# Kernel optimization log

Hardware: AMD Instinct MI355X
Metric: run time of the kernel (lower is better)

## Reference

```python
import jax, jax.numpy as jnp
import numpy as np


def setup_inputs() -> dict:
    key = jax.random.key(0)
    L, N, Q, C = 6, 64, 64, 256
    hs_pair = jax.random.normal(key, (L, N, Q, C), dtype=jnp.float32)
    return {"hs_pair": hs_pair}


def _merge_step(centers):
    # centers: [L, N, Q, C] -> [L, N, Q-1, C]
    L, N, Q, C = centers.shape
    # pairwise Euclidean distance via gram matrix (avoids [L,N,Q,Q,C] diff tensor)
    sq = jnp.sum(centers * centers, axis=-1)                      # [L,N,Q]
    gram = jnp.einsum('lnqc,lnpc->lnqp', centers, centers)        # [L,N,Q,Q]
    d2 = sq[..., :, None] + sq[..., None, :] - 2.0 * gram
    dist = jnp.sqrt(jnp.maximum(d2, 0.0))                         # [L,N,Q,Q]
    dist = dist + jnp.max(dist) * jnp.eye(Q, dtype=dist.dtype)
    idx = jnp.argmin(dist.reshape(L, N, Q * Q), axis=2)           # [L,N]
    x, y = idx // Q, idx % Q                                      # row-major argmin => x < y
    cx = jnp.take_along_axis(centers, x[:, :, None, None], axis=2)[:, :, 0]  # [L,N,C]
    cy = jnp.take_along_axis(centers, y[:, :, None, None], axis=2)[:, :, 0]  # [L,N,C]
    merged = (cx + cy) * 0.5
    last = centers[:, :, -1]                                      # [L,N,C]
    qr = jnp.arange(Q)
    mask_x = (qr[None, None, :] == x[:, :, None])[..., None]      # [L,N,Q,1]
    mask_y = (qr[None, None, :] == y[:, :, None])[..., None]
    centers = jnp.where(mask_x, merged[:, :, None, :], centers)
    centers = jnp.where(mask_y, last[:, :, None, :], centers)
    return centers[:, :, :-1]


def reference(hs_pair):
    centers = hs_pair
    Q0 = centers.shape[2]
    # Q-2 sequential merges; each iteration has a distinct static shape,
    # so a Python loop (unrolled under jit) is the correct structure.
    for _ in range(Q0 - 2):
        centers = _merge_step(centers)
    return centers  # [L, N, 2, C]
```

## Files before the change

kernel.cpp:

```cpp
#include <hip/hip_runtime.h>
#include <stdint.h>

#define NSLICE 384
#define QMAX   64
#define CDIM   256
#define NTHR   512

#define SW(r,c) ((r)*QMAX + ((c)^(r)))
#define INF_F  __int_as_float(0x7F800000)

__device__ __forceinline__ float dpp_sum64(float v) {
#define DPP_ADD(c) v += __int_as_float(__builtin_amdgcn_update_dpp(0, __float_as_int(v), c, 0xf, 0xf, true))
    DPP_ADD(0x111);
    DPP_ADD(0x112);
    DPP_ADD(0x114);
    DPP_ADD(0x118);
    DPP_ADD(0x142);
    DPP_ADD(0x143);
#undef DPP_ADD
    return v;
}

template<int CTRL>
__device__ __forceinline__ unsigned dpp_min_step(unsigned v) {
    unsigned o = (unsigned)__builtin_amdgcn_update_dpp((int)v, (int)v, CTRL, 0xf, 0xf, false);
    return v < o ? v : v < o ? v : (o < v ? o : v);
}

template<int CTRL>
__device__ __forceinline__ unsigned dpp_min_step2(unsigned v) {
    unsigned o = (unsigned)__builtin_amdgcn_update_dpp((int)v, (int)v, CTRL, 0xf, 0xf, false);
    return o < v ? o : v;
}

__device__ __forceinline__ unsigned wave_min_bcast(unsigned v) {
    v = dpp_min_step2<0x111>(v);
    v = dpp_min_step2<0x112>(v);
    v = dpp_min_step2<0x114>(v);
    v = dpp_min_step2<0x118>(v);
    v = dpp_min_step2<0x142>(v);
    v = dpp_min_step2<0x143>(v);
    return (unsigned)__builtin_amdgcn_readlane((int)v, 63);
}

__device__ __forceinline__ unsigned oct_min_all(unsigned v) {
    v = dpp_min_step2<0xB1>(v);
    v = dpp_min_step2<0x4E>(v);
    v = dpp_min_step2<0x124>(v);
    return v;
}

__launch_bounds__(NTHR, 4)
__global__ void hca_kernel(const float* __restrict__ in, float* __restrict__ out) {
    __shared__ __align__(16) float cen[QMAX * CDIM];
    __shared__ __align__(16) float dist[QMAX * QMAX];
    unsigned long long* const scratch = (unsigned long long*)(dist + 63 * QMAX);

    const int tid  = threadIdx.x;
    const int lane = tid & 63;
    const int w    = tid >> 6;
    const int slice = blockIdx.x;
    const float* src = in + (size_t)slice * (QMAX * CDIM);
    float* dst = out + (size_t)slice * (2 * CDIM);

    {
        const float4* s4 = (const float4*)src;
        float4* c4 = (float4*)cen;
        #pragma unroll
        for (int i = 0; i < (QMAX * CDIM / 4) / NTHR; ++i)
            c4[tid + i * NTHR] = s4[tid + i * NTHR];
    }
    __syncthreads();

    {
        float4 A[8];
        #pragma unroll
        for (int r = 0; r < 8; ++r)
            A[r] = ((const float4*)(cen + (w + 8 * r) * CDIM))[lane];

        #pragma unroll
        for (int r = 0; r < 8; ++r) {
            float t = A[r].x * A[r].x;
            t = fmaf(A[r].y, A[r].y, t); t = fmaf(A[r].z, A[r].z, t); t = fmaf(A[r].w, A[r].w, t);
            float s = dpp_sum64(t);
            if (lane == 63) dist[(w + 8 * r) * QMAX] = s;
        }
        __syncthreads();

        float sqq[8];
        #pragma unroll
        for (int r = 0; r < 8; ++r) sqq[r] = dist[(w + 8 * r) * QMAX];
        for (int p = 1; p < QMAX; ++p) {
            const float4 b = ((const float4*)(cen + p * CDIM))[lane];
            const float sqp = dist[p * QMAX];
            #pragma unroll
            for (int r = 0; r < 8; ++r) {
                const int q = w + 8 * r;
                if (q < p) {
                    float t = A[r].x * b.x;
                    t = fmaf(A[r].y, b.y, t); t = fmaf(A[r].z, b.z, t); t = fmaf(A[r].w, b.w, t);
                    float s = dpp_sum64(t);
                    if (lane == 63) {
                        float d2 = sqq[r] + sqp - 2.0f * s;
                        float d  = sqrtf(fmaxf(d2, 0.0f));
                        dist[SW(q, p)] = d;
                        dist[SW(p, q)] = d;
                    }
                }
            }
        }
    }
    __syncthreads();

    auto chunk_min = [&](const float4& dv, unsigned& part) {
        unsigned u0 = __float_as_uint(dv.x), u1 = __float_as_uint(dv.y);
        unsigned u2 = __float_as_uint(dv.z), u3 = __float_as_uint(dv.w);
        unsigned m01 = u0 < u1 ? u0 : u1;
        unsigned m23 = u2 < u3 ? u2 : u3;
        unsigned m = m01 < m23 ? m01 : m23;
        part = part < m ? part : m;
    };
    auto chunk_idx = [&](int i, const float4& dv, unsigned g, unsigned& bi) {
        const int rr  = 4 * i + (lane >> 4);
        const int rb  = rr * 64;
        const int cc0 = (lane & 15) * 4;
        #pragma unroll
        for (int e = 0; e < 4; ++e) {
            unsigned db  = __float_as_uint((&dv.x)[e]);
            unsigned idx = (unsigned)(rb + ((cc0 + e) ^ rr));
            if (db == g) bi = idx < bi ? idx : bi;
        }
    };

    unsigned flat0, d0bits;
    {
        unsigned part = 0xFFFFFFFFu;
        float4 dv[16];
        #pragma unroll
        for (int i = 0; i < 16; ++i) {
            dv[i] = ((const float4*)dist)[i * 64 + lane];
            chunk_min(dv[i], part);
        }
        d0bits = wave_min_bcast(part);
        unsigned bi = 0xFFFFFFFFu;
        #pragma unroll
        for (int i = 0; i < 16; ++i) chunk_idx(i, dv[i], d0bits, bi);
        flat0 = wave_min_bcast(bi);
    }
    __syncthreads();

    for (int Q = QMAX; Q > 2; --Q) {
        const int Qm1 = Q - 1;

        int x = 0, y = 0;
        float dxy = 0.0f;
        if (w < 2) {
            unsigned flat, g;
            if (Q == QMAX) {
                flat = flat0; g = d0bits;
            } else {
                unsigned long long k = scratch[lane & 7];
                unsigned hi = (unsigned)(k >> 32), lo = (unsigned)k;
                g = oct_min_all(hi);
                unsigned c2 = (hi == g) ? lo : 0xFFFFFFFFu;
                flat = oct_min_all(c2);
            }
            x = (int)((flat >> 6) & 63); y = (int)(flat & 63);
            dxy = __uint_as_float(g);
        }

        if (w == 0) {
            const int p = lane;
            const bool act = (p < Qm1) && (p != x);
            const int p_old = (p == y) ? Qm1 : p;
            float dxp = 0.0f, dyp = 0.0f;
            if (act) { dxp = dist[SW(x, p_old)]; dyp = dist[SW(y, p_old)]; }
            const bool mv = (y != Qm1) && (p < Qm1) && (p != x) && (p != y);
            float rowQ1 = 0.0f, colQ1 = 0.0f;
            if (mv) { rowQ1 = dist[SW(Qm1, p)]; colQ1 = dist[SW(p, Qm1)]; }
            float t = 0.5f * (dxp * dxp + dyp * dyp) - 0.25f * (dxy * dxy);
            float d = sqrtf(fmaxf(t, 0.0f));
            if (mv) { dist[SW(y, p)] = rowQ1; dist[SW(p, y)] = colQ1; }
            if (p < Q) { dist[SW(Qm1, p)] = INF_F; dist[SW(p, Qm1)] = INF_F; }
            if (act) { dist[SW(x, p)] = d; dist[SW(p, x)] = d; }
        }
        if (w == 1) {
            const float4 cx  = ((const float4*)(cen + x * CDIM))[lane];
            const float4 cy4 = ((const float4*)(cen + y * CDIM))[lane];
            const float4 cq  = ((const float4*)(cen + Qm1 * CDIM))[lane];
            float4 m;
            m.x = (cx.x + cy4.x) * 0.5f; m.y = (cx.y + cy4.y) * 0.5f;
            m.z = (cx.z + cy4.z) * 0.5f; m.w = (cx.w + cy4.w) * 0.5f;
            ((float4*)(cen + x * CDIM))[lane] = m;
            if (y != Qm1) ((float4*)(cen + y * CDIM))[lane] = cq;
        }
        __syncthreads();

        if (Q > 3) {
            const int Qs = Q - 1;
            unsigned part = 0xFFFFFFFFu;
            float4 v0, v1;
            const bool l0 = (4 * w < Qs);
            const bool l1 = (4 * (w + 8) < Qs);
            if (l0) {
                v0 = ((const float4*)dist)[w * 64 + lane];
                chunk_min(v0, part);
            }
            if (l1) {
                v1 = ((const float4*)dist)[(w + 8) * 64 + lane];
                if (w + 8 == 15 && lane >= 48) {
                    v1.x = INF_F; v1.y = INF_F; v1.z = INF_F; v1.w = INF_F;
                }
                chunk_min(v1, part);
            }
            unsigned g = wave_min_bcast(part);
            unsigned bi = 0xFFFFFFFFu;
            if (l0) chunk_idx(w, v0, g, bi);
            if (l1) chunk_idx(w + 8, v1, g, bi);
            unsigned bidx = wave_min_bcast(bi);
            if (lane == 0) scratch[w] = ((unsigned long long)g << 32) | bidx;
        }
        __syncthreads();
    }

    for (int i = tid; i < 2 * CDIM; i += NTHR)
        dst[i] = cen[i];
}

extern "C" void kernel_launch(void* const* d_in, const int* in_sizes, int n_in,
                              void* d_out, int out_size, void* d_ws, size_t ws_size,
                              hipStream_t stream) {
    (void)in_sizes; (void)n_in; (void)d_ws; (void)ws_size; (void)out_size;
    const float* in = (const float*)d_in[0];
    float* out = (float*)d_out;
    hca_kernel<<<NSLICE, NTHR, 0, stream>>>(in, out);
}
```

Before: 127.9 us.

## Halve block to four waves and reduce candidates with scalar 64-bit min

Cuts the workgroup from 8 to 4 waves, so each wave now holds 16 rows in the Gram phase and scans 4 float4 chunks per step of the sequential argmin loop. The cross-wave combine now reads the four scratch entries as packed 64-bit keys and takes their min directly, replacing the octet DPP reductions, then broadcasts x, y and dxy with readfirstlane. The aim is to cut per-iteration barrier and reduction overhead in the 62-step serial loop, since fewer waves take part in each __syncthreads. The cost is more register pressure and more serial work per wave in the Gram phase.

```diff
diff --git a/kernel.cpp b/kernel.cpp
--- a/kernel.cpp
+++ b/kernel.cpp
@@ -4,10 +4,11 @@
 #define NSLICE 384
 #define QMAX   64
 #define CDIM   256
-#define NTHR   512
+#define NTHR   256
 
 #define SW(r,c) ((r)*QMAX + ((c)^(r)))
 #define INF_F  __int_as_float(0x7F800000)
+typedef unsigned long long ull;
 
 __device__ __forceinline__ float dpp_sum64(float v) {
 #define DPP_ADD(c) v += __int_as_float(__builtin_amdgcn_update_dpp(0, __float_as_int(v), c, 0xf, 0xf, true))
@@ -24,37 +25,24 @@
 template<int CTRL>
 __device__ __forceinline__ unsigned dpp_min_step(unsigned v) {
     unsigned o = (unsigned)__builtin_amdgcn_update_dpp((int)v, (int)v, CTRL, 0xf, 0xf, false);
-    return v < o ? v : v < o ? v : (o < v ? o : v);
-}
-
-template<int CTRL>
-__device__ __forceinline__ unsigned dpp_min_step2(unsigned v) {
-    unsigned o = (unsigned)__builtin_amdgcn_update_dpp((int)v, (int)v, CTRL, 0xf, 0xf, false);
     return o < v ? o : v;
 }
 
 __device__ __forceinline__ unsigned wave_min_bcast(unsigned v) {
-    v = dpp_min_step2<0x111>(v);
-    v = dpp_min_step2<0x112>(v);
-    v = dpp_min_step2<0x114>(v);
-    v = dpp_min_step2<0x118>(v);
-    v = dpp_min_step2<0x142>(v);
-    v = dpp_min_step2<0x143>(v);
+    v = dpp_min_step<0x111>(v);
+    v = dpp_min_step<0x112>(v);
+    v = dpp_min_step<0x114>(v);
+    v = dpp_min_step<0x118>(v);
+    v = dpp_min_step<0x142>(v);
+    v = dpp_min_step<0x143>(v);
     return (unsigned)__builtin_amdgcn_readlane((int)v, 63);
 }
 
-__device__ __forceinline__ unsigned oct_min_all(unsigned v) {
-    v = dpp_min_step2<0xB1>(v);
-    v = dpp_min_step2<0x4E>(v);
-    v = dpp_min_step2<0x124>(v);
-    return v;
-}
-
-__launch_bounds__(NTHR, 4)
+__launch_bounds__(NTHR, 2)
 __global__ void hca_kernel(const float* __restrict__ in, float* __restrict__ out) {
     __shared__ __align__(16) float cen[QMAX * CDIM];
     __shared__ __align__(16) float dist[QMAX * QMAX];
-    unsigned long long* const scratch = (unsigned long long*)(dist + 63 * QMAX);
+    ull* const scratch = (ull*)(dist + 63 * QMAX);
 
     const int tid  = threadIdx.x;
     const int lane = tid & 63;
@@ -73,29 +61,29 @@
     __syncthreads();
 
     {
-        float4 A[8];
-        #pragma unroll
-        for (int r = 0; r < 8; ++r)
-            A[r] = ((const float4*)(cen + (w + 8 * r) * CDIM))[lane];
-
-        #pragma unroll
-        for (int r = 0; r < 8; ++r) {
+        float4 A[16];
+        #pragma unroll
+        for (int r = 0; r < 16; ++r)
+            A[r] = ((const float4*)(cen + (w + 4 * r) * CDIM))[lane];
+
+        #pragma unroll
+        for (int r = 0; r < 16; ++r) {
             float t = A[r].x * A[r].x;
             t = fmaf(A[r].y, A[r].y, t); t = fmaf(A[r].z, A[r].z, t); t = fmaf(A[r].w, A[r].w, t);
             float s = dpp_sum64(t);
-            if (lane == 63) dist[(w + 8 * r) * QMAX] = s;
+            if (lane == 63) dist[(w + 4 * r) * QMAX] = s;
         }
         __syncthreads();
 
-        float sqq[8];
-        #pragma unroll
-        for (int r = 0; r < 8; ++r) sqq[r] = dist[(w + 8 * r) * QMAX];
+        float sqq[16];
+        #pragma unroll
+        for (int r = 0; r < 16; ++r) sqq[r] = dist[(w + 4 * r) * QMAX];
         for (int p = 1; p < QMAX; ++p) {
             const float4 b = ((const float4*)(cen + p * CDIM))[lane];
             const float sqp = dist[p * QMAX];
             #pragma unroll
-            for (int r = 0; r < 8; ++r) {
-                const int q = w + 8 * r;
+            for (int r = 0; r < 16; ++r) {
+                const int q = w + 4 * r;
                 if (q < p) {
                     float t = A[r].x * b.x;
                     t = fmaf(A[r].y, b.y, t); t = fmaf(A[r].z, b.z, t); t = fmaf(A[r].w, b.w, t);
@@ -155,18 +143,20 @@
         int x = 0, y = 0;
         float dxy = 0.0f;
         if (w < 2) {
-            unsigned flat, g;
+            ull kmin;
             if (Q == QMAX) {
-                flat = flat0; g = d0bits;
+                kmin = ((ull)d0bits << 32) | flat0;
             } else {
-                unsigned long long k = scratch[lane & 7];
-                unsigned hi = (unsigned)(k >> 32), lo = (unsigned)k;
-                g = oct_min_all(hi);
-                unsigned c2 = (hi == g) ? lo : 0xFFFFFFFFu;
-                flat = oct_min_all(c2);
+                ull s0 = scratch[0], s1 = scratch[1], s2 = scratch[2], s3 = scratch[3];
+                ull a0 = s0 < s1 ? s0 : s1;
+                ull a1 = s2 < s3 ? s2 : s3;
+                kmin = a0 < a1 ? a0 : a1;
             }
-            x = (int)((flat >> 6) & 63); y = (int)(flat & 63);
-            dxy = __uint_as_float(g);
+            const unsigned fl = (unsigned)kmin & 0xFFFu;
+            x = __builtin_amdgcn_readfirstlane((int)(fl >> 6));
+            y = __builtin_amdgcn_readfirstlane((int)(fl & 63u));
+            dxy = __uint_as_float(
+                (unsigned)__builtin_amdgcn_readfirstlane((int)(unsigned)(kmin >> 32)));
         }
 
         if (w == 0) {
@@ -199,32 +189,34 @@
         if (Q > 3) {
             const int Qs = Q - 1;
             unsigned part = 0xFFFFFFFFu;
-            float4 v0, v1;
-            const bool l0 = (4 * w < Qs);
-            const bool l1 = (4 * (w + 8) < Qs);
-            if (l0) {
-                v0 = ((const float4*)dist)[w * 64 + lane];
-                chunk_min(v0, part);
-            }
-            if (l1) {
-                v1 = ((const float4*)dist)[(w + 8) * 64 + lane];
-                if (w + 8 == 15 && lane >= 48) {
-                    v1.x = INF_F; v1.y = INF_F; v1.z = INF_F; v1.w = INF_F;
+            float4 v[4];
+            bool lv[4];
+            #pragma unroll
+            for (int j = 0; j < 4; ++j) {
+                const int c = w + 4 * j;
+                lv[j] = (4 * c < Qs);
+                if (lv[j]) {
+                    v[j] = ((const float4*)dist)[c * 64 + lane];
+                    if (c == 15 && lane >= 48) {
+                        v[j].x = INF_F; v[j].y = INF_F; v[j].z = INF_F; v[j].w = INF_F;
+                    }
+                    chunk_min(v[j], part);
                 }
-                chunk_min(v1, part);
             }
             unsigned g = wave_min_bcast(part);
             unsigned bi = 0xFFFFFFFFu;
-            if (l0) chunk_idx(w, v0, g, bi);
-            if (l1) chunk_idx(w + 8, v1, g, bi);
+            #pragma unroll
+            for (int j = 0; j < 4; ++j)
+                if (lv[j]) chunk_idx(w + 4 * j, v[j], g, bi);
             unsigned bidx = wave_min_bcast(bi);
-            if (lane == 0) scratch[w] = ((unsigned long long)g << 32) | bidx;
+            if (lane == 0) scratch[w] = ((ull)g << 32) | bidx;
         }
         __syncthreads();
     }
 
-    for (int i = tid; i < 2 * CDIM; i += NTHR)
-        dst[i] = cen[i];
+    #pragma unroll
+    for (int i = 0; i < 2; ++i)
+        dst[tid + i * NTHR] = cen[tid + i * NTHR];
 }
 
 extern "C" void kernel_launch(void* const* d_in, const int* in_sizes, int n_in,
```

Result: slower. 160.4 us (+25.4%).
